# Optimization experiments

Measured on AMD Instinct MI355X. Metric: run time of the kernel, lower is better.

Reference implementation:

```python
import jax, jax.numpy as jnp
import numpy as np

B, S, A, M, H, OUT = 256, 256, 256, 256, 8, 256
KD = A // H   # key_dim per head = 32
VD = M // H   # value_dim per head = 32


def setup_inputs() -> dict:
    key = jax.random.key(0)
    ks = jax.random.split(key, 11)
    return {
        "q_data": jax.random.normal(ks[0], (B, S, A), dtype=jnp.float32),
        "m_data": jax.random.normal(ks[1], (B, S, M), dtype=jnp.float32),
        "bias": jax.random.normal(ks[2], (B, 1, 1, S), dtype=jnp.float32),
        "nonbatched_bias": jax.random.normal(ks[3], (H, S, S), dtype=jnp.float32),
        "query_w": jax.random.normal(ks[4], (A, H, KD), dtype=jnp.float32) * 0.05,
        "key_w": jax.random.normal(ks[5], (M, H, KD), dtype=jnp.float32) * 0.05,
        "value_w": jax.random.normal(ks[6], (M, H, VD), dtype=jnp.float32) * 0.05,
        "gating_w": jax.random.normal(ks[7], (A, H, VD), dtype=jnp.float32) * 0.05,
        "gating_b": jax.random.normal(ks[8], (H, VD), dtype=jnp.float32) * 0.05,
        "output_w": jax.random.normal(ks[9], (H, VD, OUT), dtype=jnp.float32) * 0.05,
        "output_b": jax.random.normal(ks[10], (OUT,), dtype=jnp.float32) * 0.05,
    }


def reference(q_data, m_data, bias, nonbatched_bias,
              query_w, key_w, value_w, gating_w, gating_b, output_w, output_b):
    key_dim = query_w.shape[-1]
    # projections
    q = jnp.einsum('bqa,ahc->bqhc', q_data, query_w) * key_dim ** (-0.5)
    k = jnp.einsum('bka,ahc->bkhc', m_data, key_w)
    v = jnp.einsum('bka,ahc->bkhc', m_data, value_w)
    # logits [b,h,q,k] with batched + shared bias
    logits = jnp.einsum('bqhc,bkhc->bhqk', q, k) + bias + nonbatched_bias[None]
    weights = jax.nn.softmax(logits, axis=-1)
    weighted_avg = jnp.einsum('bhqk,bkhc->bqhc', weights, v)
    # sigmoid gating
    gate_values = jax.nn.sigmoid(jnp.einsum('bqc,chv->bqhv', q_data, gating_w) + gating_b)
    weighted_avg = weighted_avg * gate_values
    # output projection
    output = jnp.einsum('bqhc,hco->bqo', weighted_avg, output_w) + output_b
    return output
```

## Files before the change

kernel.cpp:

```cpp
#include <hip/hip_runtime.h>

typedef unsigned short u16;
typedef __attribute__((ext_vector_type(8))) short short8;
typedef __attribute__((ext_vector_type(4))) float f32x4;
typedef __attribute__((ext_vector_type(4))) unsigned int u32x4;
typedef __attribute__((ext_vector_type(4))) unsigned short u16x4;

#define LOG2E 1.4426950408889634f

__device__ __forceinline__ float bf2f(u16 u) {
    union { float f; unsigned int i; } c; c.i = ((unsigned int)u) << 16; return c.f;
}
__device__ __forceinline__ u16 f2bf(float f) {
    unsigned int x = __float_as_uint(f);
    x += 0x7fff + ((x >> 16) & 1);
    return (u16)(x >> 16);
}
__device__ __forceinline__ unsigned int cvtpk(float lo, float hi) {
    unsigned int d;
    asm("v_cvt_pk_bf16_f32 %0, %1, %2" : "=v"(d) : "v"(lo), "v"(hi));
    return d;
}

union Cvt32 { u32x4 v[4]; u16 u[32]; };

__device__ __forceinline__ void ld32f_bf(const float* __restrict__ p, Cvt32& t) {
    union { unsigned int i[8]; u32x4 v[2]; } a;
#pragma unroll
    for (int j = 0; j < 4; j++) {
        f32x4 x = *(const f32x4*)(p + j * 4);
        a.i[j * 2]     = cvtpk(x[0], x[1]);
        a.i[j * 2 + 1] = cvtpk(x[2], x[3]);
    }
    t.v[0] = a.v[0]; t.v[1] = a.v[1];
#pragma unroll
    for (int j = 0; j < 4; j++) {
        f32x4 x = *(const f32x4*)(p + 16 + j * 4);
        a.i[j * 2]     = cvtpk(x[0], x[1]);
        a.i[j * 2 + 1] = cvtpk(x[2], x[3]);
    }
    t.v[2] = a.v[0]; t.v[3] = a.v[1];
}


__global__ __launch_bounds__(256) void prep_a(
    const float* __restrict__ nb,
    const float* __restrict__ qw, const float* __restrict__ kw,
    const float* __restrict__ vw, const float* __restrict__ gw,
    const float* __restrict__ ow,
    u16* __restrict__ wt, u16* __restrict__ WoT, u16* __restrict__ nbT)
{
    __shared__ float tile[64][65];
    int blk = blockIdx.x, tid = threadIdx.x;
    if (blk < 1024) {
        int i = blk * 256 + tid;
        int half = i >> 17;
        int rem = i & 131071;
        int h = rem >> 14, e = rem & 16383;
        int n = e >> 8, k = e & 255;
        int src_idx = k * 256 + h * 32 + (n & 31);
        float v;
        if (half == 0) v = (n < 32) ? kw[src_idx] : vw[src_idx];
        else           v = (n < 32) ? qw[src_idx] : gw[src_idx];
        wt[i] = f2bf(v);
    } else if (blk < 1280) {
        int e = (blk - 1024) * 256 + tid;
        int o = e & 255, hc = e >> 8;
        WoT[o * 256 + hc] = f2bf(ow[hc * 256 + o]);
    } else {
        int idx = blk - 1280;
        int q0 = (idx & 3) * 64, k0 = ((idx >> 2) & 3) * 64, h = idx >> 4;
        int rr = tid >> 4;
        int cc = (tid & 15) << 2;
        const float* src = nb + ((size_t)(h * 256 + q0)) * 256 + k0;
#pragma unroll
        for (int p = 0; p < 4; p++) {
            int q = rr + p * 16;
            f32x4 x = *(const f32x4*)(src + (size_t)q * 256 + cc);
            tile[q][cc] = x[0]; tile[q][cc + 1] = x[1];
            tile[q][cc + 2] = x[2]; tile[q][cc + 3] = x[3];
        }
        __syncthreads();
        u16* dst = nbT + ((size_t)(h * 256 + k0)) * 256 + q0;
#pragma unroll
        for (int p = 0; p < 4; p++) {
            int k = rr + p * 16;
            u16x4 o;
#pragma unroll
            for (int u = 0; u < 4; u++) o[u] = f2bf(tile[cc + u][k] * LOG2E);
            *(u16x4*)(dst + (size_t)k * 256 + cc) = o;
        }
    }
}

__global__ __launch_bounds__(256) void fusedA(
    const float* __restrict__ q_data, const float* __restrict__ m_data,
    const float* __restrict__ bias2, const u16* __restrict__ nbT,
    const u16* __restrict__ wt, const float* __restrict__ gb,
    u16* __restrict__ WA)
{
    __shared__ u16 smem[23296];
    u16* Vt  = smem;
    u16* Xs  = smem + 8448;
    u16* Ksh = Xs;
    u16* Wsh = smem + 18688;

    int bid = blockIdx.x;
    int xcd = bid & 7;
    int j = bid >> 3;
    int h = j & 7;
    int b = (xcd << 5) | (j >> 3);
    int tid = threadIdx.x, lane = tid & 63, w = tid >> 6;
    int l15 = lane & 15;
    int kl = (lane >> 4) << 3;
    int rq = (lane >> 4) << 2;
    const f32x4 fz = {0.f, 0.f, 0.f, 0.f};

    float bload[16];
#pragma unroll
    for (int t = 0; t < 16; t++)
        bload[t] = bias2[(b << 8) + t * 16 + l15] * LOG2E;
    float gbc0 = gb[h * 32 + l15];
    float gbc1 = gb[h * 32 + 16 + l15];

    int srow = tid >> 1;
    int sc16 = (tid & 1) << 4;
    int nrow = tid >> 1, nc = (tid & 1) << 4;

    const float* Xg2 = q_data + ((size_t)b << 16);
    const u16* Wg2 = wt + 131072 + (h << 14);
    f32x4 acc2[4][4];
#pragma unroll
    for (int i = 0; i < 4; i++)
#pragma unroll
        for (int j2 = 0; j2 < 4; j2++) acc2[i][j2] = fz;

    for (int kb = 0; kb < 8; ++kb) {
        u32x4 c0[2], c1[2];
#pragma unroll
        for (int p = 0; p < 2; ++p) {
            const float* ps = Xg2 + (size_t)(p * 128 + srow) * 256 + kb * 32 + sc16;
            f32x4 x0 = *(const f32x4*)ps;
            f32x4 x1 = *(const f32x4*)(ps + 4);
            f32x4 x2 = *(const f32x4*)(ps + 8);
            f32x4 x3 = *(const f32x4*)(ps + 12);
            union { unsigned int i4[4]; u32x4 v; } a, c;
            a.i4[0] = cvtpk(x0[0], x0[1]); a.i4[1] = cvtpk(x0[2], x0[3]);
            a.i4[2] = cvtpk(x1[0], x1[1]); a.i4[3] = cvtpk(x1[2], x1[3]);
            c.i4[0] = cvtpk(x2[0], x2[1]); c.i4[1] = cvtpk(x2[2], x2[3]);
            c.i4[2] = cvtpk(x3[0], x3[1]); c.i4[3] = cvtpk(x3[2], x3[3]);
            c0[p] = a.v; c1[p] = c.v;
        }
        u32x4 b0, b1;
        if (tid < 128) {
            const u16* q = Wg2 + nrow * 256 + kb * 32 + nc;
            b0 = *(const u32x4*)q; b1 = *(const u32x4*)(q + 8);
        }
        if (kb) __syncthreads();
#pragma unroll
        for (int p = 0; p < 2; ++p) {
            int row = p * 128 + srow;
            *(u32x4*)&Xs[row * 40 + sc16]     = c0[p];
            *(u32x4*)&Xs[row * 40 + sc16 + 8] = c1[p];
        }
        if (tid < 128) {
            *(u32x4*)&Wsh[nrow * 40 + nc] = b0;
            *(u32x4*)&Wsh[nrow * 40 + nc + 8] = b1;
        }
        __syncthreads();
        short8 af[4], bf[4];
#pragma unroll
        for (int i = 0; i < 4; i++) af[i] = *(const short8*)&Xs[(64 * w + i * 16 + l15) * 40 + kl];
#pragma unroll
        for (int i = 0; i < 4; i++) bf[i] = *(const short8*)&Wsh[(i * 16 + l15) * 40 + kl];
#pragma unroll
        for (int mi = 0; mi < 4; mi++)
#pragma unroll
            for (int ni = 0; ni < 4; ni++)
                acc2[mi][ni] = __builtin_amdgcn_mfma_f32_16x16x32_bf16(af[mi], bf[ni], acc2[mi][ni], 0, 0, 0);
    }

    const float* Xg = m_data + ((size_t)b << 16);
    const u16* Wg = wt + (h << 14);
    f32x4 acc[4][4];
#pragma unroll
    for (int i = 0; i < 4; i++)
#pragma unroll
        for (int j2 = 0; j2 < 4; j2++) acc[i][j2] = fz;

    for (int kb = 0; kb < 8; ++kb) {
        u32x4 c0[2], c1[2];
#pragma unroll
        for (int p = 0; p < 2; ++p) {
            const float* ps = Xg + (size_t)(p * 128 + srow) * 256 + kb * 32 + sc16;
            f32x4 x0 = *(const f32x4*)ps;
            f32x4 x1 = *(const f32x4*)(ps + 4);
            f32x4 x2 = *(const f32x4*)(ps + 8);
            f32x4 x3 = *(const f32x4*)(ps + 12);
            union { unsigned int i4[4]; u32x4 v; } a, c;
            a.i4[0] = cvtpk(x0[0], x0[1]); a.i4[1] = cvtpk(x0[2], x0[3]);
            a.i4[2] = cvtpk(x1[0], x1[1]); a.i4[3] = cvtpk(x1[2], x1[3]);
            c.i4[0] = cvtpk(x2[0], x2[1]); c.i4[1] = cvtpk(x2[2], x2[3]);
            c.i4[2] = cvtpk(x3[0], x3[1]); c.i4[3] = cvtpk(x3[2], x3[3]);
            c0[p] = a.v; c1[p] = c.v;
        }
        u32x4 b0, b1;
        if (tid < 128) {
            const u16* q = Wg + nrow * 256 + kb * 32 + nc;
            b0 = *(const u32x4*)q; b1 = *(const u32x4*)(q + 8);
        }
        __syncthreads();
#pragma unroll
        for (int p = 0; p < 2; ++p) {
            int row = p * 128 + srow;
            *(u32x4*)&Xs[row * 40 + sc16]     = c0[p];
            *(u32x4*)&Xs[row * 40 + sc16 + 8] = c1[p];
        }
        if (tid < 128) {
            *(u32x4*)&Wsh[nrow * 40 + nc] = b0;
            *(u32x4*)&Wsh[nrow * 40 + nc + 8] = b1;
        }
        __syncthreads();
        short8 af[4], bf[4];
#pragma unroll
        for (int i = 0; i < 4; i++) af[i] = *(const short8*)&Xs[(64 * w + i * 16 + l15) * 40 + kl];
#pragma unroll
        for (int i = 0; i < 4; i++) bf[i] = *(const short8*)&Wsh[(i * 16 + l15) * 40 + kl];
#pragma unroll
        for (int mi = 0; mi < 4; mi++)
#pragma unroll
            for (int ni = 0; ni < 4; ni++)
                acc[mi][ni] = __builtin_amdgcn_mfma_f32_16x16x32_bf16(af[mi], bf[ni], acc[mi][ni], 0, 0, 0);
    }
#pragma unroll
    for (int mi = 0; mi < 4; mi++)
#pragma unroll
        for (int ni = 0; ni < 4; ni++)
#pragma unroll
            for (int r = 0; r < 4; r++) {
                int s = 64 * w + mi * 16 + rq + r;
                int col = ni * 16 + l15;
                u16 v = f2bf(acc[mi][ni][r]);
                if (ni < 2) Ksh[s * 40 + col] = v;
                else        Vt[(col - 32) * 264 + s] = v;
            }
    __syncthreads();

    u16* myQP = smem + 18688 + w * 1152;
    const u16* nbh = nbT + ((size_t)h << 16);
    const float qs = 0.17677669529663687f * LOG2E;
    int orow = lane >> 2, ocol = (lane & 3) << 3;

#pragma unroll
    for (int mt = 0; mt < 4; ++mt) {
        int q0 = 64 * w + mt * 16 + rq;
#pragma unroll
        for (int ni = 0; ni < 2; ++ni)
#pragma unroll
            for (int r = 0; r < 4; r++)
                myQP[(rq + r) * 40 + ni * 16 + l15] = f2bf(acc2[mt][ni][r] * qs);
        short8 qf = *(const short8*)&myQP[l15 * 40 + kl];

        const u16* nbp = nbh + q0;
        float srow_[4] = {0.f, 0.f, 0.f, 0.f};
        f32x4 oacc[2] = {fz, fz};
#pragma unroll
        for (int qt = 0; qt < 4; ++qt) {
            f32x4 sc[4];
#pragma unroll
            for (int t = 0; t < 4; t++) {
                int tt = qt * 4 + t;
                short8 kfr = *(const short8*)&Ksh[(tt * 16 + l15) * 40 + kl];
                f32x4 cb = {bload[tt], bload[tt], bload[tt], bload[tt]};
                sc[t] = __builtin_amdgcn_mfma_f32_16x16x32_bf16(qf, kfr, cb, 0, 0, 0);
            }
#pragma unroll
            for (int t = 0; t < 4; t++) {
                int tt = qt * 4 + t;
                u16x4 nbv = *(const u16x4*)(nbp + ((tt * 16 + l15) << 8));
#pragma unroll
                for (int r = 0; r < 4; r++) {
                    float p = __builtin_amdgcn_exp2f(sc[t][r] + bf2f(nbv[r]));
                    srow_[r] += p;
                    myQP[(rq + r) * 72 + t * 16 + l15] = f2bf(p);
                }
            }
#pragma unroll
            for (int ks = 0; ks < 2; ++ks) {
                short8 pf = *(const short8*)&myQP[l15 * 72 + ks * 32 + kl];
#pragma unroll
                for (int ni = 0; ni < 2; ++ni) {
                    short8 vf = *(const short8*)&Vt[(ni * 16 + l15) * 264 + qt * 64 + ks * 32 + kl];
                    oacc[ni] = __builtin_amdgcn_mfma_f32_16x16x32_bf16(pf, vf, oacc[ni], 0, 0, 0);
                }
            }
        }
#pragma unroll
        for (int r = 0; r < 4; r++) {
            float s = srow_[r];
            s += __shfl_xor(s, 1);
            s += __shfl_xor(s, 2);
            s += __shfl_xor(s, 4);
            s += __shfl_xor(s, 8);
            srow_[r] = __builtin_amdgcn_rcpf(s);
        }

#pragma unroll
        for (int ni = 0; ni < 2; ++ni) {
            float gbv = ni ? gbc1 : gbc0;
#pragma unroll
            for (int r = 0; r < 4; r++) {
                float gate = __builtin_amdgcn_rcpf(
                    1.f + __builtin_amdgcn_exp2f(-(acc2[mt][ni + 2][r] + gbv) * LOG2E));
                myQP[(rq + r) * 40 + ni * 16 + l15] = f2bf(oacc[ni][r] * srow_[r] * gate);
            }
        }
        u32x4 ov = *(const u32x4*)&myQP[orow * 40 + ocol];
        *(u32x4*)(WA + ((size_t)((b << 8) + 64 * w + mt * 16 + orow) << 8) + h * 32 + ocol) = ov;
    }
}

__global__ __launch_bounds__(256) void gemmout_a(
    const u16* __restrict__ WA, const u16* __restrict__ WoT,
    float* __restrict__ dst, const float* __restrict__ ob)
{
    __shared__ u16 As[128 * 40];
    __shared__ u16 Bs[128 * 40];
    int bid = blockIdx.x;
    int xcd = bid & 7;
    int s = bid >> 3;
    int y = s & 1;
    int x = (xcd << 6) | (s >> 1);
    int row0 = x * 128;
    int n0 = y * 128;

    int tid = threadIdx.x;
    int lane = tid & 63, w = tid >> 6;
    int wm = w >> 1, wn = w & 1;
    int lr = tid >> 1;
    int lc = (tid & 1) << 4;

    const f32x4 fz = {0.f, 0.f, 0.f, 0.f};
    f32x4 acc[4][4];
#pragma unroll
    for (int i = 0; i < 4; i++)
#pragma unroll
        for (int j = 0; j < 4; j++) acc[i][j] = fz;

    int kl = (lane >> 4) << 3;
    int l15 = lane & 15;
    int rm = wm * 64 + l15;
    int rn = wn * 64 + l15;

    for (int kb = 0; kb < 8; ++kb) {
        int k0 = kb << 5;
        const u16* pa = WA + ((size_t)(row0 + lr) << 8) + k0 + lc;
        u32x4 a0 = *(const u32x4*)pa;
        u32x4 a1 = *(const u32x4*)(pa + 8);
        const u16* pb = WoT + ((size_t)(n0 + lr) << 8) + k0 + lc;
        u32x4 b0 = *(const u32x4*)pb;
        u32x4 b1 = *(const u32x4*)(pb + 8);
        if (kb) __syncthreads();
        *(u32x4*)&As[lr * 40 + lc] = a0;
        *(u32x4*)&As[lr * 40 + lc + 8] = a1;
        *(u32x4*)&Bs[lr * 40 + lc] = b0;
        *(u32x4*)&Bs[lr * 40 + lc + 8] = b1;
        __syncthreads();
        short8 af[4], bf[4];
#pragma unroll
        for (int i = 0; i < 4; i++) af[i] = *(const short8*)&As[(rm + i * 16) * 40 + kl];
#pragma unroll
        for (int i = 0; i < 4; i++) bf[i] = *(const short8*)&Bs[(rn + i * 16) * 40 + kl];
#pragma unroll
        for (int mi = 0; mi < 4; mi++)
#pragma unroll
            for (int ni = 0; ni < 4; ni++)
                acc[mi][ni] = __builtin_amdgcn_mfma_f32_16x16x32_bf16(af[mi], bf[ni], acc[mi][ni], 0, 0, 0);
    }

#pragma unroll
    for (int mi = 0; mi < 4; mi++)
#pragma unroll
        for (int ni = 0; ni < 4; ni++)
#pragma unroll
            for (int r = 0; r < 4; r++) {
                int row = row0 + wm * 64 + mi * 16 + ((lane >> 4) << 2) + r;
                int col = n0 + wn * 64 + ni * 16 + l15;
                dst[((size_t)row << 8) + col] = acc[mi][ni][r] + ob[col];
            }
}


__global__ __launch_bounds__(256) void transpose_k(
    const float* __restrict__ query_w, const float* __restrict__ key_w,
    const float* __restrict__ value_w, const float* __restrict__ gating_w,
    u16* __restrict__ wt)
{
    int i = blockIdx.x * 256 + threadIdx.x;
    int half = i >> 17;
    int rem = i & 131071;
    int h = rem >> 14, e = rem & 16383;
    int n = e >> 8, k = e & 255;
    int src_idx = k * 256 + h * 32 + (n & 31);
    float v;
    if (half == 0) v = (n < 32) ? key_w[src_idx]   : value_w[src_idx];
    else           v = (n < 32) ? query_w[src_idx] : gating_w[src_idx];
    wt[i] = f2bf(v);
}

__global__ __launch_bounds__(256) void fused_attn_k(
    const float* __restrict__ q_data, const float* __restrict__ m_data,
    const float* __restrict__ bias2, const float* __restrict__ nb,
    const u16* __restrict__ wt, const float* __restrict__ gb,
    u16* __restrict__ WAo)
{
    __shared__ u16 smem[31488];
    u16* Ksh = smem;
    u16* Vt  = smem + 10240;
    u16* Xs  = smem + 18688;
    u16* Wsh = smem + 28928;

    int bid = blockIdx.x;
    int b = bid >> 3, h = bid & 7;
    int tid = threadIdx.x, lane = tid & 63, w = tid >> 6;
    int l15 = lane & 15;
    int kl = (lane >> 4) << 3;
    int rq = (lane >> 4) << 2;
    const f32x4 fz = {0.f, 0.f, 0.f, 0.f};

    float bload[16];
#pragma unroll
    for (int t = 0; t < 16; t++) bload[t] = bias2[(b << 8) + t * 16 + l15];
    float gbc0 = gb[h * 32 + l15];
    float gbc1 = gb[h * 32 + 16 + l15];

    const float* Xg = m_data + ((size_t)b << 16);
    const u16* Wg = wt + (h << 14);
    f32x4 acc[4][4];
#pragma unroll
    for (int i = 0; i < 4; i++)
#pragma unroll
        for (int j = 0; j < 4; j++) acc[i][j] = fz;

    for (int kb = 0; kb < 8; ++kb) {
        Cvt32 am;
        ld32f_bf(Xg + (size_t)tid * 256 + kb * 32, am);
        u32x4 b0, b1;
        int nrow = tid >> 1, nc = (tid & 1) << 4;
        if (tid < 128) {
            const u16* q = Wg + nrow * 256 + kb * 32 + nc;
            b0 = *(const u32x4*)q; b1 = *(const u32x4*)(q + 8);
        }
        if (kb) __syncthreads();
        *(u32x4*)&Xs[tid * 40]      = am.v[0];
        *(u32x4*)&Xs[tid * 40 + 8]  = am.v[1];
        *(u32x4*)&Xs[tid * 40 + 16] = am.v[2];
        *(u32x4*)&Xs[tid * 40 + 24] = am.v[3];
        if (tid < 128) {
            *(u32x4*)&Wsh[nrow * 40 + nc] = b0;
            *(u32x4*)&Wsh[nrow * 40 + nc + 8] = b1;
        }
        __syncthreads();
        short8 af[4], bf[4];
#pragma unroll
        for (int i = 0; i < 4; i++) af[i] = *(const short8*)&Xs[(64 * w + i * 16 + l15) * 40 + kl];
#pragma unroll
        for (int i = 0; i < 4; i++) bf[i] = *(const short8*)&Wsh[(i * 16 + l15) * 40 + kl];
#pragma unroll
        for (int mi = 0; mi < 4; mi++)
#pragma unroll
            for (int ni = 0; ni < 4; ni++)
                acc[mi][ni] = __builtin_amdgcn_mfma_f32_16x16x32_bf16(af[mi], bf[ni], acc[mi][ni], 0, 0, 0);
    }
#pragma unroll
    for (int mi = 0; mi < 4; mi++)
#pragma unroll
        for (int ni = 0; ni < 4; ni++)
#pragma unroll
            for (int r = 0; r < 4; r++) {
                int s = 64 * w + mi * 16 + rq + r;
                int col = ni * 16 + l15;
                u16 v = f2bf(acc[mi][ni][r]);
                if (ni < 2) Ksh[s * 40 + col] = v;
                else        Vt[(col - 32) * 264 + s] = v;
            }
    __syncthreads();

    const float* Xg2 = q_data + ((size_t)b << 16);
    const u16* Wg2 = wt + 131072 + (h << 14);
    f32x4 acc2[4][4];
#pragma unroll
    for (int i = 0; i < 4; i++)
#pragma unroll
        for (int j = 0; j < 4; j++) acc2[i][j] = fz;

    for (int kb = 0; kb < 8; ++kb) {
        Cvt32 am;
        ld32f_bf(Xg2 + (size_t)tid * 256 + kb * 32, am);
        u32x4 b0, b1;
        int nrow = tid >> 1, nc = (tid & 1) << 4;
        if (tid < 128) {
            const u16* q = Wg2 + nrow * 256 + kb * 32 + nc;
            b0 = *(const u32x4*)q; b1 = *(const u32x4*)(q + 8);
        }
        __syncthreads();
        *(u32x4*)&Xs[tid * 40]      = am.v[0];
        *(u32x4*)&Xs[tid * 40 + 8]  = am.v[1];
        *(u32x4*)&Xs[tid * 40 + 16] = am.v[2];
        *(u32x4*)&Xs[tid * 40 + 24] = am.v[3];
        if (tid < 128) {
            *(u32x4*)&Wsh[nrow * 40 + nc] = b0;
            *(u32x4*)&Wsh[nrow * 40 + nc + 8] = b1;
        }
        __syncthreads();
        short8 af[4], bf[4];
#pragma unroll
        for (int i = 0; i < 4; i++) af[i] = *(const short8*)&Xs[(64 * w + i * 16 + l15) * 40 + kl];
#pragma unroll
        for (int i = 0; i < 4; i++) bf[i] = *(const short8*)&Wsh[(i * 16 + l15) * 40 + kl];
#pragma unroll
        for (int mi = 0; mi < 4; mi++)
#pragma unroll
            for (int ni = 0; ni < 4; ni++)
                acc2[mi][ni] = __builtin_amdgcn_mfma_f32_16x16x32_bf16(af[mi], bf[ni], acc2[mi][ni], 0, 0, 0);
    }
    __syncthreads();

    u16* myQ = smem + 18688 + w * 2816;
    u16* myP = myQ + 640;
    const float* nbp = nb + ((size_t)h << 16);
    const float qscale = 0.17677669529663687f;

#pragma unroll
    for (int mt = 0; mt < 4; ++mt) {
#pragma unroll
        for (int ni = 0; ni < 2; ++ni)
#pragma unroll
            for (int r = 0; r < 4; r++)
                myQ[(rq + r) * 40 + ni * 16 + l15] = f2bf(acc2[mt][ni][r] * qscale);

        short8 qf = *(const short8*)&myQ[l15 * 40 + kl];
        f32x4 sc[16];
#pragma unroll
        for (int t = 0; t < 16; t++) {
            short8 kfr = *(const short8*)&Ksh[(t * 16 + l15) * 40 + kl];
            sc[t] = __builtin_amdgcn_mfma_f32_16x16x32_bf16(qf, kfr, fz, 0, 0, 0);
        }

        int q0 = 64 * w + mt * 16 + rq;
        float mrow[4] = {-3e30f, -3e30f, -3e30f, -3e30f};
#pragma unroll
        for (int t = 0; t < 16; t++) {
            int kidx = t * 16 + l15;
#pragma unroll
            for (int r = 0; r < 4; r++) {
                float v = sc[t][r] + bload[t] + nbp[(size_t)(q0 + r) * 256 + kidx];
                sc[t][r] = v;
                mrow[r] = fmaxf(mrow[r], v);
            }
        }
#pragma unroll
        for (int r = 0; r < 4; r++) {
            float m = mrow[r];
            m = fmaxf(m, __shfl_xor(m, 1));
            m = fmaxf(m, __shfl_xor(m, 2));
            m = fmaxf(m, __shfl_xor(m, 4));
            m = fmaxf(m, __shfl_xor(m, 8));
            mrow[r] = m;
        }
        float srow[4] = {0.f, 0.f, 0.f, 0.f};
#pragma unroll
        for (int t = 0; t < 16; t++)
#pragma unroll
            for (int r = 0; r < 4; r++) {
                float p = __expf(sc[t][r] - mrow[r]);
                sc[t][r] = p;
                srow[r] += p;
            }
#pragma unroll
        for (int r = 0; r < 4; r++) {
            float s = srow[r];
            s += __shfl_xor(s, 1);
            s += __shfl_xor(s, 2);
            s += __shfl_xor(s, 4);
            s += __shfl_xor(s, 8);
            srow[r] = 1.f / s;
        }

        f32x4 oacc[2] = {fz, fz};
#pragma unroll
        for (int half = 0; half < 2; ++half) {
#pragma unroll
            for (int t = 0; t < 8; t++)
#pragma unroll
                for (int r = 0; r < 4; r++)
                    myP[(rq + r) * 136 + t * 16 + l15] =
                        f2bf(sc[half * 8 + t][r] * srow[r]);
#pragma unroll
            for (int ks = 0; ks < 4; ++ks) {
                short8 pf = *(const short8*)&myP[l15 * 136 + ks * 32 + kl];
#pragma unroll
                for (int ni = 0; ni < 2; ++ni) {
                    short8 vf = *(const short8*)&Vt[(ni * 16 + l15) * 264 + half * 128 + ks * 32 + kl];
                    oacc[ni] = __builtin_amdgcn_mfma_f32_16x16x32_bf16(pf, vf, oacc[ni], 0, 0, 0);
                }
            }
        }

#pragma unroll
        for (int ni = 0; ni < 2; ++ni) {
            float gbv = ni ? gbc1 : gbc0;
#pragma unroll
            for (int r = 0; r < 4; r++) {
                float gate = 1.f / (1.f + __expf(-(acc2[mt][ni + 2][r] + gbv)));
                size_t idx = (((size_t)b << 8) + q0 + r) * 256 + h * 32 + ni * 16 + l15;
                WAo[idx] = f2bf(oacc[ni][r] * gate);
            }
        }
    }
}

__global__ __launch_bounds__(256) void gemm_out_k(
    const u16* __restrict__ X, const float* __restrict__ Wo,
    float* __restrict__ dst, const float* __restrict__ cbias)
{
    __shared__ u16 As[128 * 40];
    __shared__ u16 Bs[128 * 40];
    int tid = threadIdx.x;
    int lane = tid & 63, w = tid >> 6;
    int wm = w >> 1, wn = w & 1;
    int row0 = blockIdx.x * 128;
    int n0 = blockIdx.y * 128;
    int lr = tid >> 1;
    int lc = (tid & 1) << 4;

    const f32x4 fz = {0.f, 0.f, 0.f, 0.f};
    f32x4 acc[4][4];
#pragma unroll
    for (int i = 0; i < 4; i++)
#pragma unroll
        for (int j = 0; j < 4; j++) acc[i][j] = fz;

    int kl = (lane >> 4) << 3;
    int l15 = lane & 15;
    int rm = wm * 64 + l15;
    int rn = wn * 64 + l15;

    for (int kb = 0; kb < 8; ++kb) {
        int k0 = kb << 5;
        const u16* pa = X + ((size_t)(row0 + lr) << 8) + k0 + lc;
        u32x4 a0 = *(const u32x4*)pa;
        u32x4 a1 = *(const u32x4*)(pa + 8);
        int bk = tid >> 3, bn = (tid & 7) << 4;
        const float* pb = Wo + (size_t)(k0 + bk) * 256 + n0 + bn;
        u16 bu[16];
#pragma unroll
        for (int j = 0; j < 16; j += 4) {
            f32x4 x = *(const f32x4*)(pb + j);
            bu[j] = f2bf(x[0]); bu[j + 1] = f2bf(x[1]);
            bu[j + 2] = f2bf(x[2]); bu[j + 3] = f2bf(x[3]);
        }
        if (kb) __syncthreads();
        *(u32x4*)&As[lr * 40 + lc] = a0;
        *(u32x4*)&As[lr * 40 + lc + 8] = a1;
#pragma unroll
        for (int j = 0; j < 16; j++) Bs[(bn + j) * 40 + bk] = bu[j];
        __syncthreads();
        short8 af[4], bf[4];
#pragma unroll
        for (int i = 0; i < 4; i++) af[i] = *(const short8*)&As[(rm + i * 16) * 40 + kl];
#pragma unroll
        for (int i = 0; i < 4; i++) bf[i] = *(const short8*)&Bs[(rn + i * 16) * 40 + kl];
#pragma unroll
        for (int mi = 0; mi < 4; mi++)
#pragma unroll
            for (int ni = 0; ni < 4; ni++)
                acc[mi][ni] = __builtin_amdgcn_mfma_f32_16x16x32_bf16(af[mi], bf[ni], acc[mi][ni], 0, 0, 0);
    }

#pragma unroll
    for (int mi = 0; mi < 4; mi++)
#pragma unroll
        for (int ni = 0; ni < 4; ni++)
#pragma unroll
            for (int r = 0; r < 4; r++) {
                int row = row0 + wm * 64 + mi * 16 + ((lane >> 4) << 2) + r;
                int col = n0 + wn * 64 + ni * 16 + l15;
                dst[((size_t)row << 8) + col] = acc[mi][ni][r] + cbias[col];
            }
}

extern "C" void kernel_launch(void* const* d_in, const int* in_sizes, int n_in,
                              void* d_out, int out_size, void* d_ws, size_t ws_size,
                              hipStream_t stream)
{
    const float* q_data   = (const float*)d_in[0];
    const float* m_data   = (const float*)d_in[1];
    const float* bias     = (const float*)d_in[2];
    const float* nb       = (const float*)d_in[3];
    const float* query_w  = (const float*)d_in[4];
    const float* key_w    = (const float*)d_in[5];
    const float* value_w  = (const float*)d_in[6];
    const float* gating_w = (const float*)d_in[7];
    const float* gating_b = (const float*)d_in[8];
    const float* output_w = (const float*)d_in[9];
    const float* output_b = (const float*)d_in[10];

    const size_t NEED_A = 4ull * 33554432 + 524288 + 131072 + 1048576;

    if (ws_size >= NEED_A) {
        u16* ws   = (u16*)d_ws;
        u16* WA   = ws;
        u16* wt   = WA + 16777216;
        u16* WoT  = wt + 262144;
        u16* nbT  = WoT + 65536;

        prep_a<<<1408, 256, 0, stream>>>(nb, query_w, key_w, value_w, gating_w,
                                         output_w, wt, WoT, nbT);
        fusedA<<<2048, 256, 0, stream>>>(q_data, m_data, bias, nbT, wt, gating_b, WA);
        gemmout_a<<<1024, 256, 0, stream>>>(WA, WoT, (float*)d_out, output_b);
    } else {
        u16* WAb = (u16*)d_ws;
        u16* wt  = (u16*)d_out;
        transpose_k<<<1024, 256, 0, stream>>>(query_w, key_w, value_w, gating_w, wt);
        fused_attn_k<<<2048, 256, 0, stream>>>(q_data, m_data, bias, nb, wt, gating_b, WAb);
        gemm_out_k<<<dim3(512, 2), 256, 0, stream>>>(WAb, output_w, (float*)d_out, output_b);
    }
}
```

Baseline: 371.6 us.

## Double fusedA block size to 512 threads, halving rows per wave

Launches the fused attention kernel with 512 threads (8 waves) per block. Each wave now handles 32 query rows instead of 64, so per-thread accumulators and staging loads are halved and more waves are available to hide latency. Shared memory grows to hold the extra per-wave scratch buffers. The cost is more barrier participants per block and possible occupancy limits from the larger LDS footprint.

```diff
diff --git a/kernel.cpp b/kernel.cpp
--- a/kernel.cpp
+++ b/kernel.cpp
@@ -93,13 +93,13 @@
     }
 }
 
-__global__ __launch_bounds__(256) void fusedA(
+__global__ __launch_bounds__(512) void fusedA(
     const float* __restrict__ q_data, const float* __restrict__ m_data,
     const float* __restrict__ bias2, const u16* __restrict__ nbT,
     const u16* __restrict__ wt, const float* __restrict__ gb,
     u16* __restrict__ WA)
 {
-    __shared__ u16 smem[23296];
+    __shared__ u16 smem[27904];
     u16* Vt  = smem;
     u16* Xs  = smem + 8448;
     u16* Ksh = Xs;
@@ -129,52 +129,43 @@
 
     const float* Xg2 = q_data + ((size_t)b << 16);
     const u16* Wg2 = wt + 131072 + (h << 14);
-    f32x4 acc2[4][4];
-#pragma unroll
-    for (int i = 0; i < 4; i++)
+    f32x4 acc2[2][4];
+#pragma unroll
+    for (int i = 0; i < 2; i++)
 #pragma unroll
         for (int j2 = 0; j2 < 4; j2++) acc2[i][j2] = fz;
 
     for (int kb = 0; kb < 8; ++kb) {
-        u32x4 c0[2], c1[2];
-#pragma unroll
-        for (int p = 0; p < 2; ++p) {
-            const float* ps = Xg2 + (size_t)(p * 128 + srow) * 256 + kb * 32 + sc16;
-            f32x4 x0 = *(const f32x4*)ps;
-            f32x4 x1 = *(const f32x4*)(ps + 4);
-            f32x4 x2 = *(const f32x4*)(ps + 8);
-            f32x4 x3 = *(const f32x4*)(ps + 12);
-            union { unsigned int i4[4]; u32x4 v; } a, c;
-            a.i4[0] = cvtpk(x0[0], x0[1]); a.i4[1] = cvtpk(x0[2], x0[3]);
-            a.i4[2] = cvtpk(x1[0], x1[1]); a.i4[3] = cvtpk(x1[2], x1[3]);
-            c.i4[0] = cvtpk(x2[0], x2[1]); c.i4[1] = cvtpk(x2[2], x2[3]);
-            c.i4[2] = cvtpk(x3[0], x3[1]); c.i4[3] = cvtpk(x3[2], x3[3]);
-            c0[p] = a.v; c1[p] = c.v;
-        }
+        const float* ps = Xg2 + (size_t)srow * 256 + kb * 32 + sc16;
+        f32x4 x0 = *(const f32x4*)ps;
+        f32x4 x1 = *(const f32x4*)(ps + 4);
+        f32x4 x2 = *(const f32x4*)(ps + 8);
+        f32x4 x3 = *(const f32x4*)(ps + 12);
+        union { unsigned int i4[4]; u32x4 v; } a, c;
+        a.i4[0] = cvtpk(x0[0], x0[1]); a.i4[1] = cvtpk(x0[2], x0[3]);
+        a.i4[2] = cvtpk(x1[0], x1[1]); a.i4[3] = cvtpk(x1[2], x1[3]);
+        c.i4[0] = cvtpk(x2[0], x2[1]); c.i4[1] = cvtpk(x2[2], x2[3]);
+        c.i4[2] = cvtpk(x3[0], x3[1]); c.i4[3] = cvtpk(x3[2], x3[3]);
         u32x4 b0, b1;
         if (tid < 128) {
             const u16* q = Wg2 + nrow * 256 + kb * 32 + nc;
             b0 = *(const u32x4*)q; b1 = *(const u32x4*)(q + 8);
         }
         if (kb) __syncthreads();
-#pragma unroll
-        for (int p = 0; p < 2; ++p) {
-            int row = p * 128 + srow;
-            *(u32x4*)&Xs[row * 40 + sc16]     = c0[p];
-            *(u32x4*)&Xs[row * 40 + sc16 + 8] = c1[p];
-        }
+        *(u32x4*)&Xs[srow * 40 + sc16]     = a.v;
+        *(u32x4*)&Xs[srow * 40 + sc16 + 8] = c.v;
         if (tid < 128) {
             *(u32x4*)&Wsh[nrow * 40 + nc] = b0;
             *(u32x4*)&Wsh[nrow * 40 + nc + 8] = b1;
         }
         __syncthreads();
-        short8 af[4], bf[4];
-#pragma unroll
-        for (int i = 0; i < 4; i++) af[i] = *(const short8*)&Xs[(64 * w + i * 16 + l15) * 40 + kl];
+        short8 af[2], bf[4];
+#pragma unroll
+        for (int i = 0; i < 2; i++) af[i] = *(const short8*)&Xs[(32 * w + i * 16 + l15) * 40 + kl];
 #pragma unroll
         for (int i = 0; i < 4; i++) bf[i] = *(const short8*)&Wsh[(i * 16 + l15) * 40 + kl];
 #pragma unroll
-        for (int mi = 0; mi < 4; mi++)
+        for (int mi = 0; mi < 2; mi++)
 #pragma unroll
             for (int ni = 0; ni < 4; ni++)
                 acc2[mi][ni] = __builtin_amdgcn_mfma_f32_16x16x32_bf16(af[mi], bf[ni], acc2[mi][ni], 0, 0, 0);
@@ -182,63 +173,54 @@
 
     const float* Xg = m_data + ((size_t)b << 16);
     const u16* Wg = wt + (h << 14);
-    f32x4 acc[4][4];
-#pragma unroll
-    for (int i = 0; i < 4; i++)
+    f32x4 acc[2][4];
+#pragma unroll
+    for (int i = 0; i < 2; i++)
 #pragma unroll
         for (int j2 = 0; j2 < 4; j2++) acc[i][j2] = fz;
 
     for (int kb = 0; kb < 8; ++kb) {
-        u32x4 c0[2], c1[2];
-#pragma unroll
-        for (int p = 0; p < 2; ++p) {
-            const float* ps = Xg + (size_t)(p * 128 + srow) * 256 + kb * 32 + sc16;
-            f32x4 x0 = *(const f32x4*)ps;
-            f32x4 x1 = *(const f32x4*)(ps + 4);
-            f32x4 x2 = *(const f32x4*)(ps + 8);
-            f32x4 x3 = *(const f32x4*)(ps + 12);
-            union { unsigned int i4[4]; u32x4 v; } a, c;
-            a.i4[0] = cvtpk(x0[0], x0[1]); a.i4[1] = cvtpk(x0[2], x0[3]);
-            a.i4[2] = cvtpk(x1[0], x1[1]); a.i4[3] = cvtpk(x1[2], x1[3]);
-            c.i4[0] = cvtpk(x2[0], x2[1]); c.i4[1] = cvtpk(x2[2], x2[3]);
-            c.i4[2] = cvtpk(x3[0], x3[1]); c.i4[3] = cvtpk(x3[2], x3[3]);
-            c0[p] = a.v; c1[p] = c.v;
-        }
+        const float* ps = Xg + (size_t)srow * 256 + kb * 32 + sc16;
+        f32x4 x0 = *(const f32x4*)ps;
+        f32x4 x1 = *(const f32x4*)(ps + 4);
+        f32x4 x2 = *(const f32x4*)(ps + 8);
+        f32x4 x3 = *(const f32x4*)(ps + 12);
+        union { unsigned int i4[4]; u32x4 v; } a, c;
+        a.i4[0] = cvtpk(x0[0], x0[1]); a.i4[1] = cvtpk(x0[2], x0[3]);
+        a.i4[2] = cvtpk(x1[0], x1[1]); a.i4[3] = cvtpk(x1[2], x1[3]);
+        c.i4[0] = cvtpk(x2[0], x2[1]); c.i4[1] = cvtpk(x2[2], x2[3]);
+        c.i4[2] = cvtpk(x3[0], x3[1]); c.i4[3] = cvtpk(x3[2], x3[3]);
         u32x4 b0, b1;
         if (tid < 128) {
             const u16* q = Wg + nrow * 256 + kb * 32 + nc;
             b0 = *(const u32x4*)q; b1 = *(const u32x4*)(q + 8);
         }
         __syncthreads();
-#pragma unroll
-        for (int p = 0; p < 2; ++p) {
-            int row = p * 128 + srow;
-            *(u32x4*)&Xs[row * 40 + sc16]     = c0[p];
-            *(u32x4*)&Xs[row * 40 + sc16 + 8] = c1[p];
-        }
+        *(u32x4*)&Xs[srow * 40 + sc16]     = a.v;
+        *(u32x4*)&Xs[srow * 40 + sc16 + 8] = c.v;
         if (tid < 128) {
             *(u32x4*)&Wsh[nrow * 40 + nc] = b0;
             *(u32x4*)&Wsh[nrow * 40 + nc + 8] = b1;
         }
         __syncthreads();
-        short8 af[4], bf[4];
-#pragma unroll
-        for (int i = 0; i < 4; i++) af[i] = *(const short8*)&Xs[(64 * w + i * 16 + l15) * 40 + kl];
+        short8 af[2], bf[4];
+#pragma unroll
+        for (int i = 0; i < 2; i++) af[i] = *(const short8*)&Xs[(32 * w + i * 16 + l15) * 40 + kl];
 #pragma unroll
         for (int i = 0; i < 4; i++) bf[i] = *(const short8*)&Wsh[(i * 16 + l15) * 40 + kl];
 #pragma unroll
-        for (int mi = 0; mi < 4; mi++)
+        for (int mi = 0; mi < 2; mi++)
 #pragma unroll
             for (int ni = 0; ni < 4; ni++)
                 acc[mi][ni] = __builtin_amdgcn_mfma_f32_16x16x32_bf16(af[mi], bf[ni], acc[mi][ni], 0, 0, 0);
     }
 #pragma unroll
-    for (int mi = 0; mi < 4; mi++)
+    for (int mi = 0; mi < 2; mi++)
 #pragma unroll
         for (int ni = 0; ni < 4; ni++)
 #pragma unroll
             for (int r = 0; r < 4; r++) {
-                int s = 64 * w + mi * 16 + rq + r;
+                int s = 32 * w + mi * 16 + rq + r;
                 int col = ni * 16 + l15;
                 u16 v = f2bf(acc[mi][ni][r]);
                 if (ni < 2) Ksh[s * 40 + col] = v;
@@ -252,8 +234,8 @@
     int orow = lane >> 2, ocol = (lane & 3) << 3;
 
 #pragma unroll
-    for (int mt = 0; mt < 4; ++mt) {
-        int q0 = 64 * w + mt * 16 + rq;
+    for (int mt = 0; mt < 2; ++mt) {
+        int q0 = 32 * w + mt * 16 + rq;
 #pragma unroll
         for (int ni = 0; ni < 2; ++ni)
 #pragma unroll
@@ -316,7 +298,7 @@
             }
         }
         u32x4 ov = *(const u32x4*)&myQP[orow * 40 + ocol];
-        *(u32x4*)(WA + ((size_t)((b << 8) + 64 * w + mt * 16 + orow) << 8) + h * 32 + ocol) = ov;
+        *(u32x4*)(WA + ((size_t)((b << 8) + 32 * w + mt * 16 + orow) << 8) + h * 32 + ocol) = ov;
     }
 }
 
@@ -717,7 +699,7 @@
 
         prep_a<<<1408, 256, 0, stream>>>(nb, query_w, key_w, value_w, gating_w,
                                          output_w, wt, WoT, nbT);
-        fusedA<<<2048, 256, 0, stream>>>(q_data, m_data, bias, nbT, wt, gating_b, WA);
+        fusedA<<<2048, 512, 0, stream>>>(q_data, m_data, bias, nbT, wt, gating_b, WA);
         gemmout_a<<<1024, 256, 0, stream>>>(WA, WoT, (float*)d_out, output_b);
     } else {
         u16* WAb = (u16*)d_ws;
```

Result: slower. 428.7 us (+15.4%).
